# Optimization experiments

Measured on AMD Instinct MI355X. Metric: run time of the kernel, lower is better.

The kernel has to match this reference:

```python
import jax, jax.numpy as jnp
import numpy as np

N = 65536   # collocation points
D = 2       # input dim
C = 16      # num subdomains / partitions (4x4 grid)
PH = 128    # PoU hidden dim
PNMID = 2   # PoU middle (residual) layers: depth=4 -> 2 middle
SW = 256    # subnet width
SNMID = 2   # subnet middle layers: eqx MLP depth=3 -> 2 width->width layers


def setup_inputs() -> dict:
    key = jax.random.key(0)
    ks = jax.random.split(key, 8)

    def w(k, shape, fan_in):
        return jax.random.normal(k, shape, jnp.float32) / jnp.sqrt(jnp.float32(fan_in))

    x = jax.random.uniform(ks[0], (N, D), jnp.float32)  # points in [0,1]^2
    # 4x4 grid of axis-aligned subdomains covering [0,1]^2
    g = np.linspace(0.0, 1.0, 5)
    lo = np.stack(np.meshgrid(g[:-1], g[:-1], indexing='ij'), -1).reshape(-1, 2)
    hi = np.stack(np.meshgrid(g[1:], g[1:], indexing='ij'), -1).reshape(-1, 2)
    centers = jnp.asarray((lo + hi) / 2.0, jnp.float32)  # [C, D]
    scales = jnp.asarray((hi - lo) / 2.0, jnp.float32)   # [C, D]

    return dict(
        x=x, centers=centers, scales=scales,
        pou_W0=w(ks[1], (D, PH), D), pou_b0=jnp.zeros((PH,), jnp.float32),
        pou_Wmid=w(ks[2], (PNMID, PH, PH), PH), pou_bmid=jnp.zeros((PNMID, PH), jnp.float32),
        pou_Wl=w(ks[3], (PH, C), PH), pou_bl=jnp.zeros((C,), jnp.float32),
        sub_W0=w(ks[4], (C, D, SW), D), sub_b0=jnp.zeros((C, SW), jnp.float32),
        sub_Wmid=w(ks[5], (C, SNMID, SW, SW), SW), sub_bmid=jnp.zeros((C, SNMID, SW), jnp.float32),
        sub_Wl=w(ks[6], (C, SW, 1), SW), sub_bl=jnp.zeros((C, 1), jnp.float32),
    )


def reference(x, centers, scales,
              pou_W0, pou_b0, pou_Wmid, pou_bmid, pou_Wl, pou_bl,
              sub_W0, sub_b0, sub_Wmid, sub_bmid, sub_Wl, sub_bl):
    # --- PoU gating net: residual ReLU MLP + softmax over partitions ---
    h = jax.nn.relu(x @ pou_W0 + pou_b0)                  # [N, PH]
    for l in range(pou_Wmid.shape[0]):
        h = h + jax.nn.relu(h @ pou_Wmid[l] + pou_bmid[l])
    wgt = jax.nn.softmax(h @ pou_Wl + pou_bl, axis=-1)    # [N, C] window weights

    # --- per-subdomain input normalization + batched subnet MLPs (tanh) ---
    xn = (x[None, :, :] - centers[:, None, :]) / scales[:, None, :]  # [C, N, D]
    g = jnp.tanh(jnp.einsum('cnd,cdw->cnw', xn, sub_W0) + sub_b0[:, None, :])  # [C, N, SW]
    for l in range(sub_Wmid.shape[1]):
        g = jnp.tanh(jnp.einsum('cnw,cwv->cnv', g, sub_Wmid[:, l]) + sub_bmid[:, l][:, None, :])
    u = (jnp.einsum('cnw,cwo->cno', g, sub_Wl) + sub_bl[:, None, :])[:, :, 0]  # [C, N]

    # --- windowed weighted sum:  acc_n = sum_c w[n,c] * u[c,n] ---
    acc = jnp.einsum('nc,cn->n', wgt, u)                  # [N]

    # --- ansatz: hard Dirichlet BC on the unit box: u = acc * prod_d x_d (1-x_d) ---
    return acc * jnp.prod(x * (1.0 - x), axis=-1)
```

## Files before the change

### kernel.cpp

```cpp
#include <hip/hip_runtime.h>

#define NPTS 65536
#define CC 16
#define PH 128
#define SW 256
#define MB 64
#define SP 264

typedef _Float16 half8 __attribute__((ext_vector_type(8)));
typedef _Float16 half4 __attribute__((ext_vector_type(4)));
typedef _Float16 half2 __attribute__((ext_vector_type(2)));
typedef float float4_ __attribute__((ext_vector_type(4)));
typedef float float2_ __attribute__((ext_vector_type(2)));

__device__ __forceinline__ float fast_tanh(float x) {
    float e = __builtin_amdgcn_exp2f(x * 2.8853900817779268f);
    float r = __builtin_amdgcn_rcpf(e + 1.0f);
    return fmaf(-2.0f, r, 1.0f);
}

__device__ __forceinline__ half4 pack4(float a, float b, float c, float d) {
    half2 lo = __builtin_bit_cast(half2, __builtin_amdgcn_cvt_pkrtz(a, b));
    half2 hi = __builtin_bit_cast(half2, __builtin_amdgcn_cvt_pkrtz(c, d));
    half4 h;
    h[0] = lo[0]; h[1] = lo[1]; h[2] = hi[0]; h[3] = hi[1];
    return h;
}

__global__ __launch_bounds__(256) void prep_wt(const float* __restrict__ Wmid,
                                               _Float16* __restrict__ Wt) {
    __shared__ float T[64][65];
    int b = blockIdx.x;
    int cl = b >> 4;
    int tile = b & 15;
    int w0 = (tile >> 2) * 64, v0 = (tile & 3) * 64;
    int t = threadIdx.x;
    int col = t & 63, row4 = t >> 6;
    const float* src = Wmid + ((size_t)cl << 16);
#pragma unroll
    for (int rr = 0; rr < 16; ++rr) {
        int wl = rr * 4 + row4;
        T[wl][col] = src[(size_t)(w0 + wl) * 256 + v0 + col];
    }
    __syncthreads();
    _Float16* dst = Wt + ((size_t)cl << 16);
#pragma unroll
    for (int rr = 0; rr < 16; ++rr) {
        int v = rr * 4 + row4;
        dst[(size_t)(v0 + v) * 256 + w0 + col] = (_Float16)T[col][v];
    }
}

__global__ __launch_bounds__(256) void pou_kernel(
    const float* __restrict__ x, const float* __restrict__ W0,
    const float* __restrict__ b0, const float* __restrict__ Wmid,
    const float* __restrict__ bmid, const float* __restrict__ Wl,
    const float* __restrict__ bl, float* __restrict__ wgt) {
    __shared__ float hA[64][PH + 1];
    int t = threadIdx.x;
    int p = t & 63;
    int g4 = __builtin_amdgcn_readfirstlane(t >> 6);
    int jb = g4 * 32;
    int n0 = blockIdx.x * 64;
    float x0 = x[(size_t)(n0 + p) * 2];
    float x1 = x[(size_t)(n0 + p) * 2 + 1];

#pragma unroll
    for (int jj = 0; jj < 32; ++jj) {
        int j = jb + jj;
        float a = x0 * W0[j] + x1 * W0[PH + j] + b0[j];
        hA[p][j] = a > 0.f ? a : 0.f;
    }
    __syncthreads();

    for (int l = 0; l < 2; ++l) {
        float acc[32];
#pragma unroll
        for (int jj = 0; jj < 32; ++jj) acc[jj] = bmid[l * PH + jb + jj];
        for (int k = 0; k < PH; ++k) {
            float hv = hA[p][k];
#pragma unroll
            for (int jj = 0; jj < 32; ++jj)
                acc[jj] += hv * Wmid[(l * PH + k) * PH + jb + jj];
        }
        float resv[32];
#pragma unroll
        for (int jj = 0; jj < 32; ++jj) resv[jj] = hA[p][jb + jj];
        __syncthreads();
#pragma unroll
        for (int jj = 0; jj < 32; ++jj) {
            float r = acc[jj] > 0.f ? acc[jj] : 0.f;
            hA[p][jb + jj] = resv[jj] + r;
        }
        __syncthreads();
    }

    int c4 = g4 * 4;
    float lacc[4];
#pragma unroll
    for (int cc = 0; cc < 4; ++cc) lacc[cc] = bl[c4 + cc];
    for (int k = 0; k < PH; ++k) {
        float hv = hA[p][k];
#pragma unroll
        for (int cc = 0; cc < 4; ++cc) lacc[cc] += hv * Wl[k * CC + c4 + cc];
    }
    __syncthreads();
#pragma unroll
    for (int cc = 0; cc < 4; ++cc) hA[p][c4 + cc] = lacc[cc];
    __syncthreads();

    if (t < 64) {
        float lg[CC];
#pragma unroll
        for (int c = 0; c < CC; ++c) lg[c] = hA[t][c];
        float m = lg[0];
#pragma unroll
        for (int c = 1; c < CC; ++c) m = fmaxf(m, lg[c]);
        float s = 0.f;
#pragma unroll
        for (int c = 0; c < CC; ++c) {
            lg[c] = __builtin_amdgcn_exp2f((lg[c] - m) * 1.4426950408889634f);
            s += lg[c];
        }
        float inv = 1.0f / s;
        float* wr = wgt + (size_t)(n0 + t) * CC;
#pragma unroll
        for (int c = 0; c < CC; ++c) wr[c] = lg[c] * inv;
    }
}

__global__ __launch_bounds__(256, 4) void subnet_kernel(
    const float* __restrict__ x, const float* __restrict__ centers,
    const float* __restrict__ scales, const float* __restrict__ W0,
    const float* __restrict__ b0, const _Float16* __restrict__ Wt,
    const float* __restrict__ bmid, const float* __restrict__ Wl,
    const float* __restrict__ bl, float* __restrict__ u) {
    __shared__ _Float16 g[MB * SP];
    __shared__ float xs[MB][2];
    __shared__ float part[4][MB];
    int t = threadIdx.x;
    int c = blockIdx.y;
    int n0 = blockIdx.x * MB;

    if (t < MB) {
        float xx0 = x[(size_t)(n0 + t) * 2];
        float xx1 = x[(size_t)(n0 + t) * 2 + 1];
        xs[t][0] = (xx0 - centers[c * 2]) / scales[c * 2];
        xs[t][1] = (xx1 - centers[c * 2 + 1]) / scales[c * 2 + 1];
    }
    __syncthreads();

    {
        int ln = t & 63;
        int pb = (t >> 6) * 16;
        const float* W0c = W0 + (size_t)c * 2 * SW;
        float4_ w0 = *(const float4_*)&W0c[ln * 4];
        float4_ w1 = *(const float4_*)&W0c[SW + ln * 4];
        float4_ bb = *(const float4_*)&b0[c * SW + ln * 4];
#pragma unroll 4
        for (int p = 0; p < 16; ++p) {
            float2_ xv = *(const float2_*)&xs[pb + p][0];
            float tv[4];
#pragma unroll
            for (int j = 0; j < 4; ++j)
                tv[j] = fast_tanh(fmaf(xv[0], w0[j], fmaf(xv[1], w1[j], bb[j])));
            *(half4*)&g[(pb + p) * SP + ln * 4] = pack4(tv[0], tv[1], tv[2], tv[3]);
        }
    }
    __syncthreads();

    int lane = t & 63;
    int wave = t >> 6;
    int quad = lane >> 4;
    int l16 = lane & 15;
    int mb = wave * 64;

    {
        const _Float16* Wp = Wt + (((size_t)(c * 2 + 0)) << 16);
        const _Float16* Arow = Wp + (mb + l16) * SW + quad * 8;
        float4_ acc[4][4] = {};
#pragma unroll
        for (int kt = 0; kt < 8; ++kt) {
            half8 a[4], b[4];
#pragma unroll
            for (int mt = 0; mt < 4; ++mt)
                a[mt] = *(const half8*)&Arow[mt * 16 * SW + kt * 32];
#pragma unroll
            for (int nt = 0; nt < 4; ++nt)
                b[nt] = *(const half8*)&g[(nt * 16 + l16) * SP + kt * 32 + quad * 8];
#pragma unroll
            for (int mt = 0; mt < 4; ++mt)
#pragma unroll
                for (int nt = 0; nt < 4; ++nt)
                    acc[mt][nt] = __builtin_amdgcn_mfma_f32_16x16x32_f16(
                        a[mt], b[nt], acc[mt][nt], 0, 0, 0);
        }
        __syncthreads();
        const float* bp = bmid + (c * 2 + 0) * SW + mb + quad * 4;
#pragma unroll
        for (int mt = 0; mt < 4; ++mt) {
            float4_ bias = *(const float4_*)&bp[mt * 16];
#pragma unroll
            for (int nt = 0; nt < 4; ++nt) {
                float t0 = fast_tanh(acc[mt][nt][0] + bias[0]);
                float t1 = fast_tanh(acc[mt][nt][1] + bias[1]);
                float t2 = fast_tanh(acc[mt][nt][2] + bias[2]);
                float t3 = fast_tanh(acc[mt][nt][3] + bias[3]);
                *(half4*)&g[(nt * 16 + l16) * SP + mb + mt * 16 + quad * 4] =
                    pack4(t0, t1, t2, t3);
            }
        }
        __syncthreads();
    }

    {
        const _Float16* Wp = Wt + (((size_t)(c * 2 + 1)) << 16);
        const _Float16* Arow = Wp + (mb + l16) * SW + quad * 8;
        float4_ acc[4][4] = {};
#pragma unroll
        for (int kt = 0; kt < 8; ++kt) {
            half8 a[4], b[4];
#pragma unroll
            for (int mt = 0; mt < 4; ++mt)
                a[mt] = *(const half8*)&Arow[mt * 16 * SW + kt * 32];
#pragma unroll
            for (int nt = 0; nt < 4; ++nt)
                b[nt] = *(const half8*)&g[(nt * 16 + l16) * SP + kt * 32 + quad * 8];
#pragma unroll
            for (int mt = 0; mt < 4; ++mt)
#pragma unroll
                for (int nt = 0; nt < 4; ++nt)
                    acc[mt][nt] = __builtin_amdgcn_mfma_f32_16x16x32_f16(
                        a[mt], b[nt], acc[mt][nt], 0, 0, 0);
        }
        const float* bp = bmid + (c * 2 + 1) * SW + mb + quad * 4;
        const float* wlp = Wl + c * SW + mb + quad * 4;
        float s[4] = {0.f, 0.f, 0.f, 0.f};
#pragma unroll
        for (int mt = 0; mt < 4; ++mt) {
            float4_ bias = *(const float4_*)&bp[mt * 16];
            float4_ wv = *(const float4_*)&wlp[mt * 16];
#pragma unroll
            for (int nt = 0; nt < 4; ++nt) {
                float t0 = fast_tanh(acc[mt][nt][0] + bias[0]);
                float t1 = fast_tanh(acc[mt][nt][1] + bias[1]);
                float t2 = fast_tanh(acc[mt][nt][2] + bias[2]);
                float t3 = fast_tanh(acc[mt][nt][3] + bias[3]);
                s[nt] += fmaf(t0, wv[0],
                          fmaf(t1, wv[1], fmaf(t2, wv[2], t3 * wv[3])));
            }
        }
#pragma unroll
        for (int nt = 0; nt < 4; ++nt) {
            s[nt] += __shfl_xor(s[nt], 16);
            s[nt] += __shfl_xor(s[nt], 32);
        }
        if (quad == 0) {
#pragma unroll
            for (int nt = 0; nt < 4; ++nt) part[wave][nt * 16 + l16] = s[nt];
        }
    }
    __syncthreads();
    if (t < MB) {
        float s = part[0][t] + part[1][t] + part[2][t] + part[3][t] + bl[c];
        u[(size_t)c * NPTS + n0 + t] = s;
    }
}

__global__ __launch_bounds__(256) void final_kernel(const float* __restrict__ x,
                                                    const float* __restrict__ wgt,
                                                    const float* __restrict__ u,
                                                    float* __restrict__ out) {
    int n = blockIdx.x * 256 + threadIdx.x;
    const float* wr = wgt + (size_t)n * CC;
    float s = 0.f;
#pragma unroll
    for (int c = 0; c < CC; ++c) s += wr[c] * u[(size_t)c * NPTS + n];
    float x0 = x[(size_t)n * 2], x1 = x[(size_t)n * 2 + 1];
    out[n] = s * (x0 * (1.f - x0)) * (x1 * (1.f - x1));
}

extern "C" void kernel_launch(void* const* d_in, const int* in_sizes, int n_in,
                              void* d_out, int out_size, void* d_ws, size_t ws_size,
                              hipStream_t stream) {
    const float* x = (const float*)d_in[0];
    const float* centers = (const float*)d_in[1];
    const float* scales = (const float*)d_in[2];
    const float* pou_W0 = (const float*)d_in[3];
    const float* pou_b0 = (const float*)d_in[4];
    const float* pou_Wmid = (const float*)d_in[5];
    const float* pou_bmid = (const float*)d_in[6];
    const float* pou_Wl = (const float*)d_in[7];
    const float* pou_bl = (const float*)d_in[8];
    const float* sub_W0 = (const float*)d_in[9];
    const float* sub_b0 = (const float*)d_in[10];
    const float* sub_Wmid = (const float*)d_in[11];
    const float* sub_bmid = (const float*)d_in[12];
    const float* sub_Wl = (const float*)d_in[13];
    const float* sub_bl = (const float*)d_in[14];
    float* out = (float*)d_out;

    _Float16* wt = (_Float16*)d_ws;
    float* wgt = (float*)((char*)d_ws + (4u << 20));
    float* u = (float*)((char*)d_ws + (8u << 20));

    prep_wt<<<dim3(512), dim3(256), 0, stream>>>(sub_Wmid, wt);
    pou_kernel<<<dim3(NPTS / 64), dim3(256), 0, stream>>>(
        x, pou_W0, pou_b0, pou_Wmid, pou_bmid, pou_Wl, pou_bl, wgt);
    subnet_kernel<<<dim3(NPTS / MB, CC), dim3(256), 0, stream>>>(
        x, centers, scales, sub_W0, sub_b0, wt, sub_bmid, sub_Wl, sub_bl, u);
    final_kernel<<<dim3(NPTS / 256), dim3(256), 0, stream>>>(x, wgt, u, out);
}
```

Baseline: 658.4 us.

## Fuse final weighted sum into subnet kernel via atomics, bias-initialized accumulators

The final reduction kernel is folded into the subnet kernel's epilogue. Each block multiplies its subnet output by the transposed window weight and the boundary ansatz, then atomically adds the result into the zeroed output. The gating weights are stored transposed for coalesced per-partition reads. The input normalization moves from a shared-memory staging step into registers, and MFMA accumulators start from the bias. The cost is a memset, 16 atomic adds per output, and a non-deterministic summation order.

Measured after the change: 644.4 us. 2.1% less time.

```diff
diff --git a/kernel.cpp b/kernel.cpp
--- a/kernel.cpp
+++ b/kernel.cpp
@@ -55,7 +55,7 @@
     const float* __restrict__ x, const float* __restrict__ W0,
     const float* __restrict__ b0, const float* __restrict__ Wmid,
     const float* __restrict__ bmid, const float* __restrict__ Wl,
-    const float* __restrict__ bl, float* __restrict__ wgt) {
+    const float* __restrict__ bl, float* __restrict__ wgtT) {
     __shared__ float hA[64][PH + 1];
     int t = threadIdx.x;
     int p = t & 63;
@@ -123,9 +123,9 @@
             s += lg[c];
         }
         float inv = 1.0f / s;
-        float* wr = wgt + (size_t)(n0 + t) * CC;
-#pragma unroll
-        for (int c = 0; c < CC; ++c) wr[c] = lg[c] * inv;
+#pragma unroll
+        for (int c = 0; c < CC; ++c)
+            wgtT[(size_t)c * NPTS + n0 + t] = lg[c] * inv;
     }
 }
 
@@ -134,23 +134,17 @@
     const float* __restrict__ scales, const float* __restrict__ W0,
     const float* __restrict__ b0, const _Float16* __restrict__ Wt,
     const float* __restrict__ bmid, const float* __restrict__ Wl,
-    const float* __restrict__ bl, float* __restrict__ u) {
+    const float* __restrict__ bl, const float* __restrict__ wgtT,
+    float* __restrict__ out) {
     __shared__ _Float16 g[MB * SP];
-    __shared__ float xs[MB][2];
     __shared__ float part[4][MB];
     int t = threadIdx.x;
     int c = blockIdx.y;
     int n0 = blockIdx.x * MB;
 
-    if (t < MB) {
-        float xx0 = x[(size_t)(n0 + t) * 2];
-        float xx1 = x[(size_t)(n0 + t) * 2 + 1];
-        xs[t][0] = (xx0 - centers[c * 2]) / scales[c * 2];
-        xs[t][1] = (xx1 - centers[c * 2 + 1]) / scales[c * 2 + 1];
-    }
-    __syncthreads();
-
     {
+        float cx0 = centers[c * 2], cx1 = centers[c * 2 + 1];
+        float is0 = 1.0f / scales[c * 2], is1 = 1.0f / scales[c * 2 + 1];
         int ln = t & 63;
         int pb = (t >> 6) * 16;
         const float* W0c = W0 + (size_t)c * 2 * SW;
@@ -159,11 +153,13 @@
         float4_ bb = *(const float4_*)&b0[c * SW + ln * 4];
 #pragma unroll 4
         for (int p = 0; p < 16; ++p) {
-            float2_ xv = *(const float2_*)&xs[pb + p][0];
+            float2_ xv = *(const float2_*)&x[(size_t)(n0 + pb + p) * 2];
+            float xn0 = (xv[0] - cx0) * is0;
+            float xn1 = (xv[1] - cx1) * is1;
             float tv[4];
 #pragma unroll
             for (int j = 0; j < 4; ++j)
-                tv[j] = fast_tanh(fmaf(xv[0], w0[j], fmaf(xv[1], w1[j], bb[j])));
+                tv[j] = fast_tanh(fmaf(xn0, w0[j], fmaf(xn1, w1[j], bb[j])));
             *(half4*)&g[(pb + p) * SP + ln * 4] = pack4(tv[0], tv[1], tv[2], tv[3]);
         }
     }
@@ -178,7 +174,14 @@
     {
         const _Float16* Wp = Wt + (((size_t)(c * 2 + 0)) << 16);
         const _Float16* Arow = Wp + (mb + l16) * SW + quad * 8;
-        float4_ acc[4][4] = {};
+        const float* bp = bmid + (c * 2 + 0) * SW + mb + quad * 4;
+        float4_ acc[4][4];
+#pragma unroll
+        for (int mt = 0; mt < 4; ++mt) {
+            float4_ bv = *(const float4_*)&bp[mt * 16];
+#pragma unroll
+            for (int nt = 0; nt < 4; ++nt) acc[mt][nt] = bv;
+        }
 #pragma unroll
         for (int kt = 0; kt < 8; ++kt) {
             half8 a[4], b[4];
@@ -196,16 +199,14 @@
                         a[mt], b[nt], acc[mt][nt], 0, 0, 0);
         }
         __syncthreads();
-        const float* bp = bmid + (c * 2 + 0) * SW + mb + quad * 4;
 #pragma unroll
         for (int mt = 0; mt < 4; ++mt) {
-            float4_ bias = *(const float4_*)&bp[mt * 16];
 #pragma unroll
             for (int nt = 0; nt < 4; ++nt) {
-                float t0 = fast_tanh(acc[mt][nt][0] + bias[0]);
-                float t1 = fast_tanh(acc[mt][nt][1] + bias[1]);
-                float t2 = fast_tanh(acc[mt][nt][2] + bias[2]);
-                float t3 = fast_tanh(acc[mt][nt][3] + bias[3]);
+                float t0 = fast_tanh(acc[mt][nt][0]);
+                float t1 = fast_tanh(acc[mt][nt][1]);
+                float t2 = fast_tanh(acc[mt][nt][2]);
+                float t3 = fast_tanh(acc[mt][nt][3]);
                 *(half4*)&g[(nt * 16 + l16) * SP + mb + mt * 16 + quad * 4] =
                     pack4(t0, t1, t2, t3);
             }
@@ -216,7 +217,14 @@
     {
         const _Float16* Wp = Wt + (((size_t)(c * 2 + 1)) << 16);
         const _Float16* Arow = Wp + (mb + l16) * SW + quad * 8;
-        float4_ acc[4][4] = {};
+        const float* bp = bmid + (c * 2 + 1) * SW + mb + quad * 4;
+        float4_ acc[4][4];
+#pragma unroll
+        for (int mt = 0; mt < 4; ++mt) {
+            float4_ bv = *(const float4_*)&bp[mt * 16];
+#pragma unroll
+            for (int nt = 0; nt < 4; ++nt) acc[mt][nt] = bv;
+        }
 #pragma unroll
         for (int kt = 0; kt < 8; ++kt) {
             half8 a[4], b[4];
@@ -233,19 +241,17 @@
                     acc[mt][nt] = __builtin_amdgcn_mfma_f32_16x16x32_f16(
                         a[mt], b[nt], acc[mt][nt], 0, 0, 0);
         }
-        const float* bp = bmid + (c * 2 + 1) * SW + mb + quad * 4;
         const float* wlp = Wl + c * SW + mb + quad * 4;
         float s[4] = {0.f, 0.f, 0.f, 0.f};
 #pragma unroll
         for (int mt = 0; mt < 4; ++mt) {
-            float4_ bias = *(const float4_*)&bp[mt * 16];
             float4_ wv = *(const float4_*)&wlp[mt * 16];
 #pragma unroll
             for (int nt = 0; nt < 4; ++nt) {
-                float t0 = fast_tanh(acc[mt][nt][0] + bias[0]);
-                float t1 = fast_tanh(acc[mt][nt][1] + bias[1]);
-                float t2 = fast_tanh(acc[mt][nt][2] + bias[2]);
-                float t3 = fast_tanh(acc[mt][nt][3] + bias[3]);
+                float t0 = fast_tanh(acc[mt][nt][0]);
+                float t1 = fast_tanh(acc[mt][nt][1]);
+                float t2 = fast_tanh(acc[mt][nt][2]);
+                float t3 = fast_tanh(acc[mt][nt][3]);
                 s[nt] += fmaf(t0, wv[0],
                           fmaf(t1, wv[1], fmaf(t2, wv[2], t3 * wv[3])));
             }
@@ -262,22 +268,13 @@
     }
     __syncthreads();
     if (t < MB) {
-        float s = part[0][t] + part[1][t] + part[2][t] + part[3][t] + bl[c];
-        u[(size_t)c * NPTS + n0 + t] = s;
-    }
-}
-
-__global__ __launch_bounds__(256) void final_kernel(const float* __restrict__ x,
-                                                    const float* __restrict__ wgt,
-                                                    const float* __restrict__ u,
-                                                    float* __restrict__ out) {
-    int n = blockIdx.x * 256 + threadIdx.x;
-    const float* wr = wgt + (size_t)n * CC;
-    float s = 0.f;
-#pragma unroll
-    for (int c = 0; c < CC; ++c) s += wr[c] * u[(size_t)c * NPTS + n];
-    float x0 = x[(size_t)n * 2], x1 = x[(size_t)n * 2 + 1];
-    out[n] = s * (x0 * (1.f - x0)) * (x1 * (1.f - x1));
+        int n = n0 + t;
+        float uv = part[0][t] + part[1][t] + part[2][t] + part[3][t] + bl[c];
+        float w = wgtT[(size_t)c * NPTS + n];
+        float2_ xv = *(const float2_*)&x[(size_t)n * 2];
+        float ans = (xv[0] * (1.f - xv[0])) * (xv[1] * (1.f - xv[1]));
+        atomicAdd(&out[n], uv * w * ans);
+    }
 }
 
 extern "C" void kernel_launch(void* const* d_in, const int* in_sizes, int n_in,
@@ -301,13 +298,13 @@
     float* out = (float*)d_out;
 
     _Float16* wt = (_Float16*)d_ws;
-    float* wgt = (float*)((char*)d_ws + (4u << 20));
-    float* u = (float*)((char*)d_ws + (8u << 20));
-
+    float* wgtT = (float*)((char*)d_ws + (4u << 20));
+
+    hipMemsetAsync(out, 0, (size_t)out_size * sizeof(float), stream);
     prep_wt<<<dim3(512), dim3(256), 0, stream>>>(sub_Wmid, wt);
     pou_kernel<<<dim3(NPTS / 64), dim3(256), 0, stream>>>(
-        x, pou_W0, pou_b0, pou_Wmid, pou_bmid, pou_Wl, pou_bl, wgt);
+        x, pou_W0, pou_b0, pou_Wmid, pou_bmid, pou_Wl, pou_bl, wgtT);
     subnet_kernel<<<dim3(NPTS / MB, CC), dim3(256), 0, stream>>>(
-        x, centers, scales, sub_W0, sub_b0, wt, sub_bmid, sub_Wl, sub_bl, u);
-    final_kernel<<<dim3(NPTS / 256), dim3(256), 0, stream>>>(x, wgt, u, out);
-}
+        x, centers, scales, sub_W0, sub_b0, wt, sub_bmid, sub_Wl, sub_bl,
+        wgtT, out);
+}
```
